# Performance work log

Hardware: AMD Instinct MI355X
Metric: run time of the kernel (lower is better)

## Reference

```python
import jax, jax.numpy as jnp
import numpy as np

B, T, C = 2, 2048, 2048
NH, NKV = 16, 4
HD = C // NH  # 128


def setup_inputs() -> dict:
    key = jax.random.key(0)
    ks = jax.random.split(key, 5)
    w = lambda k, shape: jax.random.normal(k, shape, jnp.float32) * 0.02
    return {
        "x": jax.random.normal(ks[0], (B, T, C), jnp.float32),
        "Wq": w(ks[1], (C, C)),
        "Wk": w(ks[2], (C, NKV * HD)),
        "Wv": w(ks[3], (C, NKV * HD)),
        "Wproj": w(ks[4], (C, C)),
    }


def _rope(x):
    # x: [B, H, T, D]; rotate-half RoPE with base 10000
    D = x.shape[-1]
    t = x.shape[-2]
    inv_freq = 1.0 / (10000.0 ** (jnp.arange(0, D, 2, dtype=jnp.float32) / D))
    freqs = jnp.arange(t, dtype=jnp.float32)[:, None] * inv_freq[None, :]  # [T, D/2]
    emb = jnp.concatenate([freqs, freqs], axis=-1)  # [T, D]
    cos, sin = jnp.cos(emb), jnp.sin(emb)
    x1, x2 = x[..., : D // 2], x[..., D // 2 :]
    rotated = jnp.concatenate([-x2, x1], axis=-1)
    return x * cos + rotated * sin


def reference(x, Wq, Wk, Wv, Wproj):
    b, t, c = x.shape
    q = (x @ Wq).reshape(b, t, NH, HD).transpose(0, 2, 1, 3)    # [B,NH,T,HD]
    k = (x @ Wk).reshape(b, t, NKV, HD).transpose(0, 2, 1, 3)   # [B,NKV,T,HD]
    v = (x @ Wv).reshape(b, t, NKV, HD).transpose(0, 2, 1, 3)
    q = _rope(q)
    k = _rope(k)
    rep = NH // NKV
    k = jnp.repeat(k, rep, axis=1)  # [B,NH,T,HD]
    v = jnp.repeat(v, rep, axis=1)
    scale = 1.0 / jnp.sqrt(jnp.float32(HD))
    scores = jnp.einsum("bhqd,bhkd->bhqk", q, k) * scale        # [B,NH,T,T]
    causal = jnp.tril(jnp.ones((t, t), dtype=bool))
    scores = jnp.where(causal, scores, jnp.finfo(scores.dtype).min)
    attn = jax.nn.softmax(scores, axis=-1)
    y = jnp.einsum("bhqk,bhkd->bhqd", attn, v)                  # [B,NH,T,HD]
    y = y.transpose(0, 2, 1, 3).reshape(b, t, c)
    return y @ Wproj
```

## Files before the change

### kernel.cpp

```cpp
#include <hip/hip_runtime.h>

#define B_ 2
#define T_ 2048
#define C_ 2048
#define NH_ 16
#define NKV_ 4
#define HD_ 128
#define M_ 4096
#define NQKV_ 3072

typedef __bf16 bf16x8 __attribute__((ext_vector_type(8)));
typedef float f32x4 __attribute__((ext_vector_type(4)));
typedef float f32x16 __attribute__((ext_vector_type(16)));

__device__ __forceinline__ unsigned short f2bf(float f) {
  union { float f; unsigned u; } c{f};
  unsigned u = c.u + 0x7FFFu + ((c.u >> 16) & 1u);
  return (unsigned short)(u >> 16);
}
__device__ __forceinline__ float bf2f(unsigned short h) {
  union { unsigned u; float f; } c{(unsigned)h << 16};
  return c.f;
}

#define GLOAD_LDS16(g, l)                                        \
  __builtin_amdgcn_global_load_lds(                              \
      (const __attribute__((address_space(1))) void*)(g),        \
      (__attribute__((address_space(3))) void*)(l), 16, 0, 0)

__device__ __forceinline__ bf16x8 ldsread128(const unsigned short* p) {
  uint4 d;
  asm volatile("ds_read_b128 %0, %1"
               : "=v"(d)
               : "v"((const __attribute__((address_space(3))) void*)p));
  union { uint4 u; bf16x8 v; } c;
  c.u = d;
  return c.v;
}

__global__ void prep_kernel(const float* __restrict__ x, const float* __restrict__ Wq,
                            const float* __restrict__ Wk, const float* __restrict__ Wv,
                            const float* __restrict__ Wp, unsigned short* __restrict__ xb,
                            unsigned short* __restrict__ wt, float2* __restrict__ rt) {
  int id = blockIdx.x;
  int t = threadIdx.x;
  if (id < 2560) {
    __shared__ float tile[64][65];
    const float* W;
    unsigned short* Wt;
    int N, bx, by;
    if (id < 1024)      { W = Wq; Wt = wt;                       N = 2048; int u = id;        bx = u & 31; by = u >> 5; }
    else if (id < 1280) { W = Wk; Wt = wt + (size_t)2048 * 2048; N = 512;  int u = id - 1024; bx = u & 7;  by = u >> 3; }
    else if (id < 1536) { W = Wv; Wt = wt + (size_t)2560 * 2048; N = 512;  int u = id - 1280; bx = u & 7;  by = u >> 3; }
    else                { W = Wp; Wt = wt + (size_t)3072 * 2048; N = 2048; int u = id - 1536; bx = u & 31; by = u >> 5; }
    const int K = 2048;
    bx *= 64; by *= 64;
    int n = t & 63, k4 = t >> 6;
#pragma unroll
    for (int r = 0; r < 16; ++r)
      tile[k4 + r * 4][n] = W[(size_t)(by + k4 + r * 4) * N + bx + n];
    __syncthreads();
    int nw = t >> 2, kb = (t & 3) * 16;
    unsigned short tmp[16];
#pragma unroll
    for (int j = 0; j < 16; ++j) tmp[j] = f2bf(tile[kb + j][nw]);
    unsigned short* dst = Wt + (size_t)(bx + nw) * K + by + kb;
#pragma unroll
    for (int j = 0; j < 2; ++j)
      *reinterpret_cast<uint4*>(dst + j * 8) = reinterpret_cast<uint4*>(tmp)[j];
  } else if (id < 10752) {
    int i = (id - 2560) * 256 + t;
    float4 v = reinterpret_cast<const float4*>(x)[i];
    union { ushort4 u; unsigned short s[4]; } o;
    o.s[0] = f2bf(v.x); o.s[1] = f2bf(v.y); o.s[2] = f2bf(v.z); o.s[3] = f2bf(v.w);
    reinterpret_cast<ushort4*>(xb)[i] = o.u;
  } else {
    int g = (id - 10752) * 256 + t;
    int tt = g >> 6, i = g & 63;
    float inv = powf(10000.f, -(float)(2 * i) / 128.f);
    float s, c;
    sincosf((float)tt * inv, &s, &c);
    rt[tt * 64 + i] = make_float2(c, s);
  }
}

template <int BM, typename OUT, bool QKV>
__global__ __launch_bounds__(512, 1) void gemm8p(const unsigned short* __restrict__ A,
                                                 const unsigned short* __restrict__ Bt,
                                                 OUT* __restrict__ Cm,
                                                 unsigned short* __restrict__ vtp,
                                                 const float2* __restrict__ rt,
                                                 int M, int N, int K) {
  constexpr int MR = BM / 64;
  __shared__ __align__(16) unsigned short As[2][2][BM * 32];
  __shared__ __align__(16) unsigned short Bs[2][2][256 * 32];
  int tid = threadIdx.x, wid = tid >> 6, lane = tid & 63;
  int l15 = lane & 15, l4 = lane >> 4;
  int wr = wid >> 1, wc = wid & 1;
  size_t arow0 = (size_t)blockIdx.y * BM;
  size_t brow0 = (size_t)blockIdx.x * 256;
  int tmax = K / 64 - 1;

  f32x4 acc[MR][8];
#pragma unroll
  for (int m = 0; m < MR; ++m)
#pragma unroll
    for (int n = 0; n < 8; ++n) acc[m][n] = (f32x4){0.f, 0.f, 0.f, 0.f};

  auto stageA = [&](int slot, int kh, int tile) {
    int k0 = tile * 64 + kh * 32;
    constexpr int NLD = (BM * 32 * 2) / (512 * 16);
#pragma unroll
    for (int i = 0; i < NLD; ++i) {
      int c = i * 512 + wid * 64 + lane;
      int rg = c >> 2, cg = (c & 3) ^ (rg & 3);
      const unsigned short* g = A + (arow0 + rg) * K + k0 + cg * 8;
      GLOAD_LDS16(g, &As[slot][kh][c * 8]);
    }
  };
  auto stageB = [&](int slot, int kh, int tile) {
    int k0 = tile * 64 + kh * 32;
#pragma unroll
    for (int i = 0; i < 2; ++i) {
      int c = i * 512 + wid * 64 + lane;
      int rg = c >> 2, cg = (c & 3) ^ (rg & 3);
      const unsigned short* g = Bt + (brow0 + rg) * K + k0 + cg * 8;
      GLOAD_LDS16(g, &Bs[slot][kh][c * 8]);
    }
  };

  stageA(0, 0, 0); stageB(0, 0, 0); stageA(0, 1, 0); stageB(0, 1, 0);
  stageA(1, 0, 1); stageB(1, 0, 1); stageA(1, 1, 1);
  if constexpr (BM == 256) asm volatile("s_waitcnt vmcnt(6)" ::: "memory");
  else                     asm volatile("s_waitcnt vmcnt(4)" ::: "memory");
  __builtin_amdgcn_s_barrier();

  int NT2 = K / 128;
  for (int it = 0; it < NT2; ++it) {
    int t2 = it * 2;
#pragma unroll
    for (int tt = 0; tt < 2; ++tt) {
      bf16x8 af[MR];
#pragma unroll
      for (int kh = 0; kh < 2; ++kh) {
#pragma unroll
        for (int nh = 0; nh < 2; ++nh) {
          int p = tt * 4 + kh * 2 + nh + 1;
          if (nh == 0) {
#pragma unroll
            for (int m = 0; m < MR; ++m) {
              int r = wr * (MR * 16) + m * 16 + l15;
              af[m] = ldsread128(&As[tt][kh][r * 32 + ((l4 ^ (r & 3)) * 8)]);
            }
          }
          bf16x8 bf[4];
#pragma unroll
          for (int j = 0; j < 4; ++j) {
            int r = wc * 128 + (nh * 4 + j) * 16 + l15;
            bf[j] = ldsread128(&Bs[tt][kh][r * 32 + ((l4 ^ (r & 3)) * 8)]);
          }
          if (p == 1) stageB(1, 1, t2 + 1);
          if (p == 2) stageA(0, 0, t2 + 2 <= tmax ? t2 + 2 : tmax);
          if (p == 3) stageB(0, 0, t2 + 2 <= tmax ? t2 + 2 : tmax);
          if (p == 4) stageA(0, 1, t2 + 2 <= tmax ? t2 + 2 : tmax);
          if (p == 5) stageB(0, 1, t2 + 2 <= tmax ? t2 + 2 : tmax);
          if (p == 6) stageA(1, 0, t2 + 3 <= tmax ? t2 + 3 : tmax);
          if (p == 7) stageB(1, 0, t2 + 3 <= tmax ? t2 + 3 : tmax);
          if (p == 8) stageA(1, 1, t2 + 3 <= tmax ? t2 + 3 : tmax);

          __builtin_amdgcn_s_barrier();
          asm volatile("s_waitcnt lgkmcnt(0)" ::: "memory");
          __builtin_amdgcn_sched_barrier(0);
          __builtin_amdgcn_s_setprio(1);
#pragma unroll
          for (int m = 0; m < MR; ++m)
#pragma unroll
            for (int j = 0; j < 4; ++j)
              acc[m][nh * 4 + j] = __builtin_amdgcn_mfma_f32_16x16x32_bf16(
                  af[m], bf[j], acc[m][nh * 4 + j], 0, 0, 0);
          __builtin_amdgcn_s_setprio(0);
          if (p == 4 || p == 8) {
            if constexpr (BM == 256) asm volatile("s_waitcnt vmcnt(6)" ::: "memory");
            else                     asm volatile("s_waitcnt vmcnt(4)" ::: "memory");
          }
          __builtin_amdgcn_s_barrier();
        }
      }
    }
  }

  if constexpr (QKV) {
    int cb = (int)(brow0 + wc * 128);
    if (cb >= 2560) {
      int kvh = (cb - 2560) >> 7;
#pragma unroll
      for (int m = 0; m < MR; ++m) {
        size_t row0 = arow0 + wr * (MR * 16) + m * 16 + l4 * 4;
        int bb = (int)(row0 >> 11), t0 = (int)(row0 & (T_ - 1));
#pragma unroll
        for (int n = 0; n < 8; ++n) {
          int d = n * 16 + l15;
          ushort4 p4;
          p4.x = f2bf(acc[m][n][0]);
          p4.y = f2bf(acc[m][n][1]);
          p4.z = f2bf(acc[m][n][2]);
          p4.w = f2bf(acc[m][n][3]);
          *reinterpret_cast<ushort4*>(
              vtp + (size_t)((bb * 4 + kvh) * 128 + d) * T_ + t0) = p4;
        }
      }
    } else {
#pragma unroll
      for (int m = 0; m < MR; ++m)
#pragma unroll
        for (int r = 0; r < 4; ++r) {
          size_t row = arow0 + wr * (MR * 16) + m * 16 + l4 * 4 + r;
          int t = (int)(row & (T_ - 1));
#pragma unroll
          for (int n = 0; n < 4; ++n) {
            float2 cs = rt[t * 64 + n * 16 + l15];
            float a1 = acc[m][n][r], a2 = acc[m][n + 4][r];
            size_t col = brow0 + wc * 128 + n * 16 + l15;
            Cm[row * N + col]      = f2bf(a1 * cs.x - a2 * cs.y);
            Cm[row * N + col + 64] = f2bf(a2 * cs.x + a1 * cs.y);
          }
        }
    }
  } else {
#pragma unroll
    for (int m = 0; m < MR; ++m)
#pragma unroll
      for (int r = 0; r < 4; ++r) {
        size_t row = arow0 + wr * (MR * 16) + m * 16 + l4 * 4 + r;
#pragma unroll
        for (int n = 0; n < 8; ++n) {
          size_t col = brow0 + wc * 128 + n * 16 + l15;
          Cm[row * N + col] = acc[m][n][r];
        }
      }
  }
}

__global__ __launch_bounds__(256, 2) void attn_kernel(const unsigned short* __restrict__ qkv,
                                                      const unsigned short* __restrict__ vt,
                                                      unsigned short* __restrict__ att,
                                                      unsigned short* __restrict__ pO,
                                                      float2* __restrict__ ml) {
  constexpr int KB = 64;
  __shared__ __align__(16) unsigned short Kl[2][KB * 128];
  __shared__ __align__(16) unsigned short Vl[2][128 * KB];
  int tid = threadIdx.x, w = tid >> 6, lane = tid & 63;
  int l31 = lane & 31, hi = lane >> 5;
  int h4 = hi * 4;

  int id = blockIdx.x;
  int qi, bh, kt0, kt1, slot = -1;
  if (id < 64) {
    qi = 9 - (id >> 5); bh = id & 31; kt0 = 0; kt1 = 2 * qi + 2;
  } else if (id < 448) {
    int s = id - 64;
    int pairidx = s >> 1, hihalf = s & 1;
    qi = 15 - (pairidx >> 5); bh = pairidx & 31;
    int nt = 2 * qi + 2, h = nt >> 1;
    kt0 = hihalf ? h : 0; kt1 = hihalf ? nt : h;
    slot = s;
  } else {
    int u = id - 448;
    qi = 7 - (u >> 5); bh = u & 31; kt0 = 0; kt1 = 2 * qi + 2;
  }
  int q0 = qi * 128;
  int b = bh >> 4, hd = bh & 15, kvh = hd >> 2;
  int qr0 = q0 + w * 32;
  int ql = qr0 + l31;

  bf16x8 qf[8];
  {
    const unsigned short* qb = qkv + (size_t)(b * T_ + ql) * NQKV_ + hd * HD_ + hi * 8;
    const float scale = 0.08838834764831845f * 1.4426950408889634f;
#pragma unroll
    for (int df = 0; df < 8; ++df) {
      bf16x8 t = *reinterpret_cast<const bf16x8*>(qb + df * 16);
#pragma unroll
      for (int j = 0; j < 8; ++j) t[j] = (__bf16)((float)t[j] * scale);
      qf[df] = t;
    }
  }

  f32x16 o[4];
#pragma unroll
  for (int dt = 0; dt < 4; ++dt)
#pragma unroll
    for (int r = 0; r < 16; ++r) o[dt][r] = 0.f;
  float mr = -1e30f, lr = 0.f;

  auto stage = [&](int buf, int kv0) {
#pragma unroll
    for (int i = 0; i < 4; ++i) {
      int c = (i * 4 + w) * 64 + lane;
      int g = c ^ ((c >> 4) & 7);
      const unsigned short* src =
          qkv + (size_t)(b * T_ + kv0 + (g >> 4)) * NQKV_ + C_ + kvh * HD_ + (g & 15) * 8;
      GLOAD_LDS16(src, &Kl[buf][(i * 4 + w) * 512]);
    }
#pragma unroll
    for (int i = 0; i < 4; ++i) {
      int c = (i * 4 + w) * 64 + lane;
      int g = c ^ ((c >> 3) & 7);
      const unsigned short* src =
          vt + (size_t)((b * NKV_ + kvh) * HD_ + (g >> 3)) * T_ + kv0 + (g & 7) * 8;
      GLOAD_LDS16(src, &Vl[buf][(i * 4 + w) * 512]);
    }
  };

  stage(0, kt0 * KB);
  __syncthreads();
  int cur = 0;
  for (int kt = kt0; kt < kt1; ++kt) {
    int kv0 = kt * KB;
    if (kt + 1 < kt1) stage(cur ^ 1, kv0 + KB);

    if (kv0 <= qr0 + 31) {
      f32x16 s[2];
#pragma unroll
      for (int r = 0; r < 16; ++r) { s[0][r] = 0.f; s[1][r] = 0.f; }
      const unsigned short* Kb = &Kl[cur][0];
      __builtin_amdgcn_s_setprio(1);
#pragma unroll
      for (int t2 = 0; t2 < 2; ++t2)
#pragma unroll
        for (int df = 0; df < 8; ++df) {
          bf16x8 kf = *reinterpret_cast<const bf16x8*>(
              Kb + (((t2 * 32 + l31) * 128 + df * 16 + hi * 8) ^ ((l31 & 7) << 3)));
          s[t2] = __builtin_amdgcn_mfma_f32_32x32x16_bf16(kf, qf[df], s[t2], 0, 0, 0);
        }
      __builtin_amdgcn_s_setprio(0);

      float rm = -1e30f;
      if ((kv0 + KB - 1) > qr0) {
#pragma unroll
        for (int t2 = 0; t2 < 2; ++t2)
#pragma unroll
          for (int r = 0; r < 16; ++r) {
            float sv = s[t2][r];
            int kcol = kv0 + t2 * 32 + (r & 3) + 8 * (r >> 2) + h4;
            if (kcol > ql) sv = -1e30f;
            s[t2][r] = sv;
            rm = fmaxf(rm, sv);
          }
      } else {
#pragma unroll
        for (int t2 = 0; t2 < 2; ++t2)
#pragma unroll
          for (int r = 0; r < 16; ++r) rm = fmaxf(rm, s[t2][r]);
      }
      rm = fmaxf(rm, __shfl_xor(rm, 32));

      if (!__all(rm <= mr + 11.0f)) {
        float mnew = fmaxf(mr, rm);
        float alpha = exp2f(mr - mnew);
        mr = mnew;
        lr *= alpha;
#pragma unroll
        for (int dt = 0; dt < 4; ++dt)
#pragma unroll
          for (int r = 0; r < 16; ++r) o[dt][r] *= alpha;
      }

      float ps = 0.f;
#pragma unroll
      for (int t2 = 0; t2 < 2; ++t2)
#pragma unroll
        for (int r = 0; r < 16; ++r) {
          float p = exp2f(s[t2][r] - mr);
          s[t2][r] = p;
          ps += p;
        }
      lr += ps;

      unsigned pk[2][8];
#pragma unroll
      for (int t2 = 0; t2 < 2; ++t2)
#pragma unroll
        for (int i = 0; i < 8; ++i) {
          union { unsigned u32; __bf16 hh[2]; } pr;
          pr.hh[0] = (__bf16)s[t2][2 * i];
          pr.hh[1] = (__bf16)s[t2][2 * i + 1];
          pk[t2][i] = pr.u32;
        }

      bf16x8 pb[4];
#pragma unroll
      for (int f = 0; f < 4; ++f) {
        int t2 = f >> 1, bq = (f & 1) * 4;
        union { bf16x8 v; unsigned d[4]; } fr;
#pragma unroll
        for (int p = 0; p < 2; ++p) {
          unsigned uu = pk[t2][bq + p];
          unsigned ww = pk[t2][bq + 2 + p];
          unsigned us = (unsigned)__shfl_xor((int)uu, 32);
          unsigned ws = (unsigned)__shfl_xor((int)ww, 32);
          fr.d[p]     = hi ? ws : uu;
          fr.d[2 + p] = hi ? ww : us;
        }
        pb[f] = fr.v;
      }

      const unsigned short* Vb = &Vl[cur][0];
      __builtin_amdgcn_s_setprio(1);
#pragma unroll
      for (int dt = 0; dt < 4; ++dt)
#pragma unroll
        for (int kf = 0; kf < 4; ++kf) {
          bf16x8 vf = *reinterpret_cast<const bf16x8*>(
              Vb + (((dt * 32 + l31) * KB + kf * 16 + hi * 8) ^ ((l31 & 7) << 3)));
          o[dt] = __builtin_amdgcn_mfma_f32_32x32x16_bf16(vf, pb[kf], o[dt], 0, 0, 0);
        }
      __builtin_amdgcn_s_setprio(0);
    }

    __syncthreads();
    cur ^= 1;
  }

  float ls = lr + __shfl_xor(lr, 32);
  if (slot < 0) {
    float inv = 1.f / ls;
    unsigned short* ob = att + (size_t)(b * T_ + ql) * C_ + hd * HD_;
#pragma unroll
    for (int dt = 0; dt < 4; ++dt)
#pragma unroll
      for (int r = 0; r < 16; ++r) {
        int d = dt * 32 + (r & 3) + 8 * (r >> 2) + h4;
        ob[d] = f2bf(o[dt][r] * inv);
      }
  } else {
    int lrow = w * 32 + l31;
    unsigned short* po = pO + (size_t)slot * 16384 + lrow * 128;
#pragma unroll
    for (int dt = 0; dt < 4; ++dt)
#pragma unroll
      for (int r = 0; r < 16; ++r) {
        int d = dt * 32 + (r & 3) + 8 * (r >> 2) + h4;
        po[d] = f2bf(o[dt][r]);
      }
    if (hi == 0) ml[slot * 128 + lrow] = make_float2(mr, ls);
  }
}

__global__ void combine_kernel(const unsigned short* __restrict__ pO,
                               const float2* __restrict__ ml,
                               unsigned short* __restrict__ att) {
  int pairidx = blockIdx.x;
  int qi = 15 - (pairidx >> 5), bh = pairidx & 31;
  int b = bh >> 4, hd = bh & 15;
  int q0 = qi * 128;
  int s0 = pairidx * 2, s1 = s0 + 1;
  int tid = threadIdx.x;
  int row = tid >> 1, dh = (tid & 1) * 64;
  float2 ml0 = ml[s0 * 128 + row], ml1 = ml[s1 * 128 + row];
  float m = fmaxf(ml0.x, ml1.x);
  float w0 = exp2f(ml0.x - m), w1 = exp2f(ml1.x - m);
  float inv = 1.f / (w0 * ml0.y + w1 * ml1.y);
  const unsigned short* p0 = pO + (size_t)s0 * 16384 + row * 128 + dh;
  const unsigned short* p1 = pO + (size_t)s1 * 16384 + row * 128 + dh;
  unsigned short* ob = att + (size_t)(b * T_ + q0 + row) * C_ + hd * HD_ + dh;
#pragma unroll
  for (int j = 0; j < 64; j += 4) {
    ushort4 a = *reinterpret_cast<const ushort4*>(p0 + j);
    ushort4 c = *reinterpret_cast<const ushort4*>(p1 + j);
    ushort4 r;
    r.x = f2bf((w0 * bf2f(a.x) + w1 * bf2f(c.x)) * inv);
    r.y = f2bf((w0 * bf2f(a.y) + w1 * bf2f(c.y)) * inv);
    r.z = f2bf((w0 * bf2f(a.z) + w1 * bf2f(c.z)) * inv);
    r.w = f2bf((w0 * bf2f(a.w) + w1 * bf2f(c.w)) * inv);
    *reinterpret_cast<ushort4*>(ob + j) = r;
  }
}

extern "C" void kernel_launch(void* const* d_in, const int* in_sizes, int n_in,
                              void* d_out, int out_size, void* d_ws, size_t ws_size,
                              hipStream_t stream) {
  const float* x  = (const float*)d_in[0];
  const float* Wq = (const float*)d_in[1];
  const float* Wk = (const float*)d_in[2];
  const float* Wv = (const float*)d_in[3];
  const float* Wp = (const float*)d_in[4];
  float* out = (float*)d_out;
  char* ws = (char*)d_ws;

  unsigned short* xb  = (unsigned short*)(ws);
  unsigned short* wt  = (unsigned short*)(ws + 16777216);
  unsigned short* qkv = (unsigned short*)(ws + 37748736);
  float2*         rt  = (float2*)(ws + 62914560);
  unsigned short* vt  = (unsigned short*)(ws + 63963136);
  unsigned short* att = xb;
  unsigned short* pO  = wt;
  float2*         ml  = rt;

  prep_kernel<<<dim3(11264), 256, 0, stream>>>(x, Wq, Wk, Wv, Wp, xb, wt, rt);

  gemm8p<256, unsigned short, true><<<dim3(NQKV_ / 256, M_ / 256), 512, 0, stream>>>(
      xb, wt, qkv, vt, rt, M_, NQKV_, C_);
  attn_kernel<<<dim3(704), 256, 0, stream>>>(qkv, vt, att, pO, ml);
  combine_kernel<<<dim3(192), 256, 0, stream>>>(pO, ml, att);
  gemm8p<128, float, false><<<dim3(C_ / 256, M_ / 128), 512, 0, stream>>>(
      att, wt + (size_t)3072 * 2048, out, nullptr, nullptr, M_, C_, C_);
}
```

Before: 211.6 us.

## Double attention query tile to 256 rows with 8 waves and rebalance split-KV schedule

The attention kernel now uses 512-thread blocks covering 256 query rows, so each staged K/V tile is reused by twice as many query rows. The work schedule is rebuilt with 448 blocks, splitting the larger query tiles into two KV halves. The first half now writes its unnormalized output straight into the att buffer, and the combine kernel reads it back from there instead of from a separate partial buffer. This cuts K/V global traffic and the combine kernel's reads, at the cost of coarser load balancing and higher register and LDS pressure per block at 512 threads.

```diff
diff --git a/kernel.cpp b/kernel.cpp
--- a/kernel.cpp
+++ b/kernel.cpp
@@ -241,7 +241,7 @@
   }
 }
 
-__global__ __launch_bounds__(256, 2) void attn_kernel(const unsigned short* __restrict__ qkv,
+__global__ __launch_bounds__(512, 2) void attn_kernel(const unsigned short* __restrict__ qkv,
                                                       const unsigned short* __restrict__ vt,
                                                       unsigned short* __restrict__ att,
                                                       unsigned short* __restrict__ pO,
@@ -254,21 +254,24 @@
   int h4 = hi * 4;
 
   int id = blockIdx.x;
-  int qi, bh, kt0, kt1, slot = -1;
-  if (id < 64) {
-    qi = 9 - (id >> 5); bh = id & 31; kt0 = 0; kt1 = 2 * qi + 2;
-  } else if (id < 448) {
-    int s = id - 64;
-    int pairidx = s >> 1, hihalf = s & 1;
-    qi = 15 - (pairidx >> 5); bh = pairidx & 31;
-    int nt = 2 * qi + 2, h = nt >> 1;
-    kt0 = hihalf ? h : 0; kt1 = hihalf ? nt : h;
-    slot = s;
+  int qi, bh, kt0, kt1, pair = -1, half = 0;
+  if (id < 256) {
+    qi = 7 - (id >> 6);
+    int l = id & 63; bh = l >> 1; half = l & 1;
+    pair = (7 - qi) * 32 + bh;
+  } else if (id < 320) {
+    qi = 3; int l = id - 256; bh = l >> 1; half = l & 1; pair = 128 + bh;
+  } else if (id < 352) {
+    qi = 1; bh = id - 320;
+  } else if (id < 416) {
+    qi = 2; int l = id - 352; bh = l >> 1; half = l & 1; pair = 160 + bh;
   } else {
-    int u = id - 448;
-    qi = 7 - (u >> 5); bh = u & 31; kt0 = 0; kt1 = 2 * qi + 2;
-  }
-  int q0 = qi * 128;
+    qi = 0; bh = id - 416;
+  }
+  int nt = 4 * qi + 4;
+  if (pair >= 0) { int h = nt >> 1; kt0 = half ? h : 0; kt1 = half ? nt : h; }
+  else           { kt0 = 0; kt1 = nt; }
+  int q0 = qi * 256;
   int b = bh >> 4, hd = bh & 15, kvh = hd >> 2;
   int qr0 = q0 + w * 32;
   int ql = qr0 + l31;
@@ -295,20 +298,20 @@
 
   auto stage = [&](int buf, int kv0) {
 #pragma unroll
-    for (int i = 0; i < 4; ++i) {
-      int c = (i * 4 + w) * 64 + lane;
+    for (int i = 0; i < 2; ++i) {
+      int c = (i * 8 + w) * 64 + lane;
       int g = c ^ ((c >> 4) & 7);
       const unsigned short* src =
           qkv + (size_t)(b * T_ + kv0 + (g >> 4)) * NQKV_ + C_ + kvh * HD_ + (g & 15) * 8;
-      GLOAD_LDS16(src, &Kl[buf][(i * 4 + w) * 512]);
-    }
-#pragma unroll
-    for (int i = 0; i < 4; ++i) {
-      int c = (i * 4 + w) * 64 + lane;
+      GLOAD_LDS16(src, &Kl[buf][(i * 8 + w) * 512]);
+    }
+#pragma unroll
+    for (int i = 0; i < 2; ++i) {
+      int c = (i * 8 + w) * 64 + lane;
       int g = c ^ ((c >> 3) & 7);
       const unsigned short* src =
           vt + (size_t)((b * NKV_ + kvh) * HD_ + (g >> 3)) * T_ + kv0 + (g & 7) * 8;
-      GLOAD_LDS16(src, &Vl[buf][(i * 4 + w) * 512]);
+      GLOAD_LDS16(src, &Vl[buf][(i * 8 + w) * 512]);
     }
   };
 
@@ -423,9 +426,9 @@
   }
 
   float ls = lr + __shfl_xor(lr, 32);
-  if (slot < 0) {
+  unsigned short* ob = att + (size_t)(b * T_ + ql) * C_ + hd * HD_;
+  if (pair < 0) {
     float inv = 1.f / ls;
-    unsigned short* ob = att + (size_t)(b * T_ + ql) * C_ + hd * HD_;
 #pragma unroll
     for (int dt = 0; dt < 4; ++dt)
 #pragma unroll
@@ -433,9 +436,18 @@
         int d = dt * 32 + (r & 3) + 8 * (r >> 2) + h4;
         ob[d] = f2bf(o[dt][r] * inv);
       }
+  } else if (half == 0) {
+#pragma unroll
+    for (int dt = 0; dt < 4; ++dt)
+#pragma unroll
+      for (int r = 0; r < 16; ++r) {
+        int d = dt * 32 + (r & 3) + 8 * (r >> 2) + h4;
+        ob[d] = f2bf(o[dt][r]);
+      }
+    if (hi == 0) ml[(pair * 2) * 256 + w * 32 + l31] = make_float2(mr, ls);
   } else {
     int lrow = w * 32 + l31;
-    unsigned short* po = pO + (size_t)slot * 16384 + lrow * 128;
+    unsigned short* po = pO + (size_t)pair * 32768 + lrow * 128;
 #pragma unroll
     for (int dt = 0; dt < 4; ++dt)
 #pragma unroll
@@ -443,37 +455,42 @@
         int d = dt * 32 + (r & 3) + 8 * (r >> 2) + h4;
         po[d] = f2bf(o[dt][r]);
       }
-    if (hi == 0) ml[slot * 128 + lrow] = make_float2(mr, ls);
+    if (hi == 0) ml[(pair * 2 + 1) * 256 + lrow] = make_float2(mr, ls);
   }
 }
 
 __global__ void combine_kernel(const unsigned short* __restrict__ pO,
                                const float2* __restrict__ ml,
                                unsigned short* __restrict__ att) {
-  int pairidx = blockIdx.x;
-  int qi = 15 - (pairidx >> 5), bh = pairidx & 31;
+  int pair = blockIdx.x;
+  int qi, bh;
+  if (pair < 128)      { qi = 7 - (pair >> 5); bh = pair & 31; }
+  else if (pair < 160) { qi = 3; bh = pair - 128; }
+  else                 { qi = 2; bh = pair - 160; }
   int b = bh >> 4, hd = bh & 15;
-  int q0 = qi * 128;
-  int s0 = pairidx * 2, s1 = s0 + 1;
+  int q0 = qi * 256;
   int tid = threadIdx.x;
-  int row = tid >> 1, dh = (tid & 1) * 64;
-  float2 ml0 = ml[s0 * 128 + row], ml1 = ml[s1 * 128 + row];
-  float m = fmaxf(ml0.x, ml1.x);
-  float w0 = exp2f(ml0.x - m), w1 = exp2f(ml1.x - m);
-  float inv = 1.f / (w0 * ml0.y + w1 * ml1.y);
-  const unsigned short* p0 = pO + (size_t)s0 * 16384 + row * 128 + dh;
-  const unsigned short* p1 = pO + (size_t)s1 * 16384 + row * 128 + dh;
-  unsigned short* ob = att + (size_t)(b * T_ + q0 + row) * C_ + hd * HD_ + dh;
-#pragma unroll
-  for (int j = 0; j < 64; j += 4) {
-    ushort4 a = *reinterpret_cast<const ushort4*>(p0 + j);
-    ushort4 c = *reinterpret_cast<const ushort4*>(p1 + j);
-    ushort4 r;
-    r.x = f2bf((w0 * bf2f(a.x) + w1 * bf2f(c.x)) * inv);
-    r.y = f2bf((w0 * bf2f(a.y) + w1 * bf2f(c.y)) * inv);
-    r.z = f2bf((w0 * bf2f(a.z) + w1 * bf2f(c.z)) * inv);
-    r.w = f2bf((w0 * bf2f(a.w) + w1 * bf2f(c.w)) * inv);
-    *reinterpret_cast<ushort4*>(ob + j) = r;
+#pragma unroll
+  for (int it = 0; it < 8; ++it) {
+    int row = it * 32 + (tid >> 3);
+    int cb = (tid & 7) * 16;
+    float2 ml0 = ml[(pair * 2) * 256 + row], ml1 = ml[(pair * 2 + 1) * 256 + row];
+    float m = fmaxf(ml0.x, ml1.x);
+    float w0 = exp2f(ml0.x - m), w1 = exp2f(ml1.x - m);
+    float inv = 1.f / (w0 * ml0.y + w1 * ml1.y);
+    unsigned short* ob = att + (size_t)(b * T_ + q0 + row) * C_ + hd * HD_ + cb;
+    const unsigned short* p1 = pO + (size_t)pair * 32768 + row * 128 + cb;
+#pragma unroll
+    for (int j = 0; j < 16; j += 4) {
+      ushort4 a = *reinterpret_cast<const ushort4*>(ob + j);
+      ushort4 c = *reinterpret_cast<const ushort4*>(p1 + j);
+      ushort4 r;
+      r.x = f2bf((w0 * bf2f(a.x) + w1 * bf2f(c.x)) * inv);
+      r.y = f2bf((w0 * bf2f(a.y) + w1 * bf2f(c.y)) * inv);
+      r.z = f2bf((w0 * bf2f(a.z) + w1 * bf2f(c.z)) * inv);
+      r.w = f2bf((w0 * bf2f(a.w) + w1 * bf2f(c.w)) * inv);
+      *reinterpret_cast<ushort4*>(ob + j) = r;
+    }
   }
 }
 
@@ -501,7 +518,7 @@
 
   gemm8p<256, unsigned short, true><<<dim3(NQKV_ / 256, M_ / 256), 512, 0, stream>>>(
       xb, wt, qkv, vt, rt, M_, NQKV_, C_);
-  attn_kernel<<<dim3(704), 256, 0, stream>>>(qkv, vt, att, pO, ml);
+  attn_kernel<<<dim3(448), 512, 0, stream>>>(qkv, vt, att, pO, ml);
   combine_kernel<<<dim3(192), 256, 0, stream>>>(pO, ml, att);
   gemm8p<128, float, false><<<dim3(C_ / 256, M_ / 128), 512, 0, stream>>>(
       att, wt + (size_t)3072 * 2048, out, nullptr, nullptr, M_, C_, C_);
```

Result: no change. 210.1 us (-0.7%).
